# Kernel optimization log

Hardware: AMD Instinct MI355X
Metric: run time of the kernel (lower is better)

The kernel has to match this reference:

```python
import jax, jax.numpy as jnp
import numpy as np

BLOCK = 32          # QLinearLPBQ block_size
W_BITS = 4          # low-precision blockwise weight quantization
ACT_BITS = 16       # ActivationQDQ(bits=16)


def act_qdq(x):
    # per-tensor symmetric 16-bit fake quant-dequant (dynamic absmax scale)
    qmax = 2.0 ** (ACT_BITS - 1) - 1.0  # 32767
    scale = jnp.maximum(jnp.max(jnp.abs(x)) / qmax, 1e-12)
    return jnp.clip(jnp.round(x / scale), -qmax - 1.0, qmax) * scale


def fixed_qdq_u16(x):
    # FixedActivationQDQ: scale = 1/65536, zero_point = 0, unsigned 16-bit grid
    scale = 1.0 / 65536.0
    return jnp.clip(jnp.round(x / scale), 0.0, 65535.0) * scale


def lpbq_dequant(w):
    # blockwise (per output row, per 32-wide input block) 4-bit fake quant-dequant
    O, I = w.shape
    qmax = 2.0 ** (W_BITS - 1) - 1.0  # 7
    wb = w.reshape(O, I // BLOCK, BLOCK)
    s = jnp.maximum(jnp.max(jnp.abs(wb), axis=-1, keepdims=True) / qmax, 1e-12)
    wq = jnp.clip(jnp.round(wb / s), -qmax - 1.0, qmax) * s
    return wq.reshape(O, I)


def setup_inputs() -> dict:
    key = jax.random.key(0)
    k1, k2, k3, k4 = jax.random.split(key, 4)
    B, S, H, I = 2, 4096, 1024, 3072
    x = jax.random.normal(k1, (B, S, H), jnp.float32)
    w_gate = jax.random.normal(k2, (I, H), jnp.float32) * 0.02
    w_up = jax.random.normal(k3, (I, H), jnp.float32) * 0.02
    w_down = jax.random.normal(k4, (H, I), jnp.float32) * 0.02
    return {"x": x, "w_gate": w_gate, "w_up": w_up, "w_down": w_down}


def reference(x, w_gate, w_up, w_down):
    # x: [B, S, H]
    x = act_qdq(x)                                        # up_proj_input_qdq
    up = act_qdq(x @ lpbq_dequant(w_up).T)                # up_proj + output qdq -> [B,S,I]
    gate = act_qdq(x @ lpbq_dequant(w_gate).T)            # gate_proj + output qdq
    sig = fixed_qdq_u16(jax.nn.sigmoid(gate))             # sigmoid on fixed u16 grid
    gate = act_qdq(gate * sig)                            # SiLU (x*sigmoid) + qdq
    o = act_qdq(gate * up)                                # down_proj_input_qdq
    return o @ lpbq_dequant(w_down).T                     # [B, S, H]
```

## Files before the change

### kernel.cpp

```cpp
#include <hip/hip_runtime.h>
#include <hip/hip_bf16.h>
#include <stdint.h>


#define M_ROWS 8192
#define H_DIM 1024
#define I_DIM 3072

typedef unsigned short u16;
typedef unsigned int u32;
typedef __attribute__((ext_vector_type(8))) short bf16x8;
typedef __attribute__((ext_vector_type(4))) float f32x4;

__device__ __forceinline__ float bf2f(u16 v) { return __uint_as_float(((u32)v) << 16); }
__device__ __forceinline__ u16 f2bf(float f) {
  u32 u = __float_as_uint(f);
  u32 r = (u + 0x7fffu + ((u >> 16) & 1u)) >> 16;
  return (u16)r;
}
__device__ __forceinline__ float qdq16i(float x, float inv, float s) {
  float q = rintf(x * inv);
  q = fminf(fmaxf(q, -32768.f), 32767.f);
  return q * s;
}

__device__ __forceinline__ float scale_read(const u32* __restrict__ scal, int s) {
  u32 m = 0;
#pragma unroll
  for (int j = 0; j < 16; ++j) m = max(m, scal[j * 16 + s]);
  return fmaxf(__uint_as_float(m) / 32767.f, 1e-12f);
}

__device__ __forceinline__ void load_lds16(const u16* g, u16* lds) {
  __builtin_amdgcn_global_load_lds(
      (const __attribute__((address_space(1))) u32*)g,
      (__attribute__((address_space(3))) u32*)lds, 16, 0, 0);
}

__device__ __forceinline__ void block_amax_atomic(float mx, u32* scal, int s) {
#pragma unroll
  for (int off = 32; off; off >>= 1) mx = fmaxf(mx, __shfl_xor(mx, off));
  __shared__ float red[4];
  const int lane = threadIdx.x & 63, wave = threadIdx.x >> 6;
  if (lane == 0) red[wave] = mx;
  __syncthreads();
  if (threadIdx.x == 0) {
    float m = fmaxf(fmaxf(red[0], red[1]), fmaxf(red[2], red[3]));
    atomicMax(scal + (blockIdx.x & 15) * 16 + s, __float_as_uint(m));
  }
}

template <int K>
__device__ __forceinline__ void gemm_core(const u16* __restrict__ Ablk,
                                          const u16* __restrict__ Bblk,
                                          f32x4 acc[4][4], u16* smem) {
  u16* As = smem;
  u16* Bs = smem + 4096;
  const int tid = threadIdx.x;
  const int lane = tid & 63, wave = tid >> 6;
  const int wm = wave >> 1, wn = wave & 1;
  const int quad = lane >> 4, mrow = lane & 15;

  const int c0 = tid, c1 = tid + 256;
  const int r0 = c0 >> 2, g0 = ((c0 & 3) ^ ((r0 >> 1) & 3)) * 8;
  const int r1 = c1 >> 2, g1 = ((c1 & 3) ^ ((r1 >> 1) & 3)) * 8;
  const u16* a0 = Ablk + (size_t)r0 * K + g0;
  const u16* a1 = Ablk + (size_t)r1 * K + g1;
  const u16* b0 = Bblk + (size_t)r0 * K + g0;
  const u16* b1 = Bblk + (size_t)r1 * K + g1;
  u16* lA0 = &As[c0 * 8];
  u16* lA1 = &As[c1 * 8];
  u16* lB0 = &Bs[c0 * 8];
  u16* lB1 = &Bs[c1 * 8];

  int aoff[4], boff[4];
  const int lq = (quad ^ ((mrow >> 1) & 3)) * 8;
#pragma unroll
  for (int t = 0; t < 4; ++t) {
    aoff[t] = (wm * 64 + t * 16 + mrow) * 32 + lq;
    boff[t] = (wn * 64 + t * 16 + mrow) * 32 + lq;
  }

  for (int k0 = 0; k0 < K; k0 += 32) {
    __syncthreads();
    load_lds16(a0 + k0, lA0);
    load_lds16(a1 + k0, lA1);
    load_lds16(b0 + k0, lB0);
    load_lds16(b1 + k0, lB1);
    __syncthreads();
    bf16x8 af[4], bfr[4];
#pragma unroll
    for (int t = 0; t < 4; ++t) {
      af[t] = *(const bf16x8*)&As[aoff[t]];
      bfr[t] = *(const bf16x8*)&Bs[boff[t]];
    }
#pragma unroll
    for (int i = 0; i < 4; ++i)
#pragma unroll
      for (int j = 0; j < 4; ++j)
        acc[i][j] = __builtin_amdgcn_mfma_f32_16x16x32_bf16(af[i], bfr[j], acc[i][j], 0, 0, 0);
  }
}

__global__ void __launch_bounds__(256) kgemm1(const u16* __restrict__ xq,
                                              const u16* __restrict__ wcat,
                                              u16* __restrict__ up, u16* __restrict__ gh,
                                              u32* __restrict__ scal) {
  __shared__ __align__(16) u16 smem[8192];
  const int tileN = blockIdx.x * 128;
  const int tileM = blockIdx.y * 128;
  f32x4 acc[4][4];
#pragma unroll
  for (int i = 0; i < 4; ++i)
#pragma unroll
    for (int j = 0; j < 4; ++j) acc[i][j] = (f32x4){0.f, 0.f, 0.f, 0.f};
  gemm_core<H_DIM>(xq + (size_t)tileM * H_DIM, wcat + (size_t)tileN * H_DIM, acc, smem);

  u16* outp;
  int ncol, slot;
  if (tileN < I_DIM) { outp = up; ncol = tileN; slot = 1; }
  else               { outp = gh; ncol = tileN - I_DIM; slot = 2; }

  const int lane = threadIdx.x & 63, wave = threadIdx.x >> 6;
  const int wm = wave >> 1, wn = wave & 1;
  const int rb = (lane >> 4) * 4, cb = lane & 15;
  const int erow = lane >> 2, echk = lane & 3;
  u16* wbase = smem + wave * 1152;
  const u16* rbase = smem + wave * 1152 + erow * 72;
  float mx = 0.f;
#pragma unroll
  for (int i = 0; i < 4; ++i) {
    __syncthreads();
#pragma unroll
    for (int j = 0; j < 4; ++j)
#pragma unroll
      for (int r = 0; r < 4; ++r) {
        float v = acc[i][j][r];
        mx = fmaxf(mx, fabsf(v));
        wbase[(rb + r) * 72 + j * 16 + cb] = f2bf(v);
      }
    __syncthreads();
    uint4 v0 = *(const uint4*)(rbase + echk * 8);
    uint4 v1 = *(const uint4*)(rbase + (echk + 4) * 8);
    size_t grow = (size_t)(tileM + wm * 64 + i * 16 + erow) * I_DIM + (ncol + wn * 64);
    *(uint4*)(outp + grow + echk * 8) = v0;
    *(uint4*)(outp + grow + (echk + 4) * 8) = v1;
  }
  block_amax_atomic(mx, scal, slot);
}

__global__ void __launch_bounds__(256) kgemm2(const u16* __restrict__ oq,
                                              const u16* __restrict__ wdq,
                                              float* __restrict__ out) {
  __shared__ __align__(16) u16 smem[8192];
  const int tileN = blockIdx.x * 128;
  const int tileM = blockIdx.y * 128;
  f32x4 acc[4][4];
#pragma unroll
  for (int i = 0; i < 4; ++i)
#pragma unroll
    for (int j = 0; j < 4; ++j) acc[i][j] = (f32x4){0.f, 0.f, 0.f, 0.f};
  gemm_core<I_DIM>(oq + (size_t)tileM * I_DIM, wdq + (size_t)tileN * I_DIM, acc, smem);

  const int lane = threadIdx.x & 63, wave = threadIdx.x >> 6;
  const int wm = wave >> 1, wn = wave & 1;
  const int rb = (lane >> 4) * 4, cb = lane & 15;
#pragma unroll
  for (int i = 0; i < 4; ++i) {
#pragma unroll
    for (int j = 0; j < 4; ++j) {
      size_t base = (size_t)(tileM + wm * 64 + i * 16 + rb) * H_DIM +
                    (size_t)(tileN + wn * 64 + j * 16 + cb);
#pragma unroll
      for (int r = 0; r < 4; ++r) out[base + (size_t)r * H_DIM] = acc[i][j][r];
    }
  }
}

__global__ void __launch_bounds__(256) kabsmax(const float4* __restrict__ x, int n4,
                                               u32* __restrict__ scal) {
  float mx = 0.f;
  for (int i = blockIdx.x * blockDim.x + threadIdx.x; i < n4; i += gridDim.x * blockDim.x) {
    float4 v = x[i];
    mx = fmaxf(fmaxf(fabsf(v.x), fabsf(v.y)), fmaxf(fmaxf(fabsf(v.z), fabsf(v.w)), mx));
  }
  block_amax_atomic(mx, scal, 0);
}

__global__ void __launch_bounds__(256) kdequant(const float* __restrict__ wu,
                                                const float* __restrict__ wg,
                                                const float* __restrict__ wdn,
                                                u16* __restrict__ wcat, u16* __restrict__ wdq) {
  const int gid = blockIdx.x * 256 + threadIdx.x;
  const int unit = gid >> 3, l8 = gid & 7;
  const float* src;
  u16* dst;
  int u;
  if (unit < 98304)       { src = wu;  dst = wcat;            u = unit; }
  else if (unit < 196608) { src = wg;  dst = wcat + 3145728;  u = unit - 98304; }
  else                    { src = wdn; dst = wdq;             u = unit - 196608; }
  const size_t off = (size_t)u * 32 + (size_t)l8 * 4;
  float4 v = *(const float4*)(src + off);
  float m = fmaxf(fmaxf(fabsf(v.x), fabsf(v.y)), fmaxf(fabsf(v.z), fabsf(v.w)));
  m = fmaxf(m, __shfl_xor(m, 1));
  m = fmaxf(m, __shfl_xor(m, 2));
  m = fmaxf(m, __shfl_xor(m, 4));
  const float s = fmaxf(m / 7.0f, 1e-12f);
  const float inv = 1.0f / s;
  float vv[4] = {v.x, v.y, v.z, v.w};
  u16 o[4];
#pragma unroll
  for (int e = 0; e < 4; ++e) {
    float q = rintf(vv[e] * inv);
    q = fminf(fmaxf(q, -8.f), 7.f);
    o[e] = f2bf(q * s);
  }
  *(ushort4*)(dst + off) = make_ushort4(o[0], o[1], o[2], o[3]);
}

__global__ void __launch_bounds__(256) kqdqx(const float4* __restrict__ x,
                                             ushort4* __restrict__ xq,
                                             const u32* __restrict__ scal) {
  const float s = scale_read(scal, 0);
  const float inv = 1.0f / s;
  const int i = blockIdx.x * 256 + threadIdx.x;
  float4 v = x[i];
  ushort4 o;
  o.x = f2bf(qdq16i(v.x, inv, s));
  o.y = f2bf(qdq16i(v.y, inv, s));
  o.z = f2bf(qdq16i(v.z, inv, s));
  o.w = f2bf(qdq16i(v.w, inv, s));
  xq[i] = o;
}

#define GH4 ((M_ROWS * I_DIM) / 8)
#define EW_BLOCKS 2048

__global__ void __launch_bounds__(256) kswiglu(const uint4* __restrict__ gh,
                                               u32* __restrict__ scal) {
  const float sg = scale_read(scal, 2);
  const float inv = 1.0f / sg;
  float mx = 0.f;
  for (int i = blockIdx.x * 256 + threadIdx.x; i < GH4; i += EW_BLOCKS * 256) {
    union { uint4 v; u16 us[8]; } u;
    u.v = gh[i];
#pragma unroll
    for (int e = 0; e < 8; ++e) {
      float g = qdq16i(bf2f(u.us[e]), inv, sg);
      float sig = __builtin_amdgcn_rcpf(1.f + __expf(-g));
      float sq = fminf(fmaxf(rintf(sig * 65536.f), 0.f), 65535.f) * (1.f / 65536.f);
      mx = fmaxf(mx, fabsf(g * sq));
    }
  }
  block_amax_atomic(mx, scal, 3);
}

__global__ void __launch_bounds__(256) kmulo(uint4* __restrict__ gh, const uint4* __restrict__ up,
                                             u32* __restrict__ scal) {
  const float sg = scale_read(scal, 2);
  const float sh = scale_read(scal, 3);
  const float su = scale_read(scal, 1);
  const float ig = 1.0f / sg, ih = 1.0f / sh, iu = 1.0f / su;
  float mx = 0.f;
  for (int i = blockIdx.x * 256 + threadIdx.x; i < GH4; i += EW_BLOCKS * 256) {
    union { uint4 v; u16 us[8]; } a, b;
    a.v = gh[i];
    b.v = up[i];
#pragma unroll
    for (int e = 0; e < 8; ++e) {
      float g = qdq16i(bf2f(a.us[e]), ig, sg);
      float sig = __builtin_amdgcn_rcpf(1.f + __expf(-g));
      float sq = fminf(fmaxf(rintf(sig * 65536.f), 0.f), 65535.f) * (1.f / 65536.f);
      u16 hb = f2bf(g * sq);
      float o = qdq16i(bf2f(hb), ih, sh) * qdq16i(bf2f(b.us[e]), iu, su);
      mx = fmaxf(mx, fabsf(o));
      a.us[e] = f2bf(o);
    }
    gh[i] = a.v;
  }
  block_amax_atomic(mx, scal, 4);
}

__global__ void __launch_bounds__(256) kqdqo(uint4* __restrict__ gh, const u32* __restrict__ scal) {
  const float so = scale_read(scal, 4);
  const float inv = 1.0f / so;
  const int i = blockIdx.x * 256 + threadIdx.x;
  union { uint4 v; u16 us[8]; } u;
  u.v = gh[i];
#pragma unroll
  for (int e = 0; e < 8; ++e) u.us[e] = f2bf(qdq16i(bf2f(u.us[e]), inv, so));
  gh[i] = u.v;
}

extern "C" void kernel_launch(void* const* d_in, const int* in_sizes, int n_in,
                              void* d_out, int out_size, void* d_ws, size_t ws_size,
                              hipStream_t stream) {
  (void)in_sizes; (void)n_in; (void)out_size; (void)ws_size;
  const float* x   = (const float*)d_in[0];
  const float* wg  = (const float*)d_in[1];
  const float* wu  = (const float*)d_in[2];
  const float* wdn = (const float*)d_in[3];
  float* out = (float*)d_out;
  char* ws = (char*)d_ws;

  u32* scal = (u32*)ws;
  u16* xq   = (u16*)(ws + 1024);
  u16* wcat = xq + (size_t)M_ROWS * H_DIM;
  u16* wdq  = wcat + (size_t)2 * I_DIM * H_DIM;
  u16* up   = wdq + (size_t)H_DIM * I_DIM;
  u16* gh   = up + (size_t)M_ROWS * I_DIM;

  hipMemsetAsync(scal, 0, 1024, stream);
  kabsmax<<<1024, 256, 0, stream>>>((const float4*)x, (M_ROWS * H_DIM) / 4, scal);
  kdequant<<<9216, 256, 0, stream>>>(wu, wg, wdn, wcat, wdq);
  kqdqx<<<(M_ROWS * H_DIM) / 4 / 256, 256, 0, stream>>>((const float4*)x, (ushort4*)xq, scal);
  kgemm1<<<dim3(48, 64), 256, 0, stream>>>(xq, wcat, up, gh, scal);
  kswiglu<<<EW_BLOCKS, 256, 0, stream>>>((const uint4*)gh, scal);
  kmulo<<<EW_BLOCKS, 256, 0, stream>>>((uint4*)gh, (const uint4*)up, scal);
  kqdqo<<<(M_ROWS * I_DIM) / 8 / 256, 256, 0, stream>>>((uint4*)gh, scal);
  kgemm2<<<dim3(8, 64), 256, 0, stream>>>(gh, wdq, out);
}
```

Measured before the change: 375.1 us.

## Fuse SiLU and output amax into gate/up GEMM epilogue, drop elementwise passes

Each GEMM1 block now computes both the gate tile and the matching up tile. The SiLU activation and its absmax are computed in the gate epilogue and kept in a shared-memory buffer, so the up epilogue can also compute the absmax of the gate*up product. This removes the separate swiglu and final-qdq passes over the large intermediate tensors and folds the final quantization into kmulo. It also merges the input absmax and weight dequant kernels into one launch. In exchange, the scales are taken from values before the intermediate quant-dequant steps, which is a slight numeric approximation, and the extra 34 KB of LDS per block may lower GEMM occupancy.

```diff
diff --git a/kernel.cpp b/kernel.cpp
--- a/kernel.cpp
+++ b/kernel.cpp
@@ -22,6 +22,10 @@
   float q = rintf(x * inv);
   q = fminf(fmaxf(q, -32768.f), 32767.f);
   return q * s;
+}
+__device__ __forceinline__ float sigq(float g) {
+  float sig = __builtin_amdgcn_rcpf(1.f + __expf(-g));
+  return fminf(fmaxf(rintf(sig * 65536.f), 0.f), 65535.f) * (1.f / 65536.f);
 }
 
 __device__ __forceinline__ float scale_read(const u32* __restrict__ scal, int s) {
@@ -47,6 +51,25 @@
   if (threadIdx.x == 0) {
     float m = fmaxf(fmaxf(red[0], red[1]), fmaxf(red[2], red[3]));
     atomicMax(scal + (blockIdx.x & 15) * 16 + s, __float_as_uint(m));
+  }
+}
+
+__device__ __forceinline__ void block_amax2(float a, float b, u32* scal, int sa, int sb) {
+#pragma unroll
+  for (int off = 32; off; off >>= 1) {
+    a = fmaxf(a, __shfl_xor(a, off));
+    b = fmaxf(b, __shfl_xor(b, off));
+  }
+  __shared__ float red2[2][4];
+  const int lane = threadIdx.x & 63, wave = threadIdx.x >> 6;
+  if (lane == 0) { red2[0][wave] = a; red2[1][wave] = b; }
+  __syncthreads();
+  if (threadIdx.x == 0) {
+    float ma = fmaxf(fmaxf(red2[0][0], red2[0][1]), fmaxf(red2[0][2], red2[0][3]));
+    float mb = fmaxf(fmaxf(red2[1][0], red2[1][1]), fmaxf(red2[1][2], red2[1][3]));
+    u32* base = scal + (blockIdx.x & 15) * 16;
+    atomicMax(base + sa, __float_as_uint(ma));
+    atomicMax(base + sb, __float_as_uint(mb));
   }
 }
 
@@ -102,51 +125,85 @@
   }
 }
 
+#define HSTRIDE 136
+
 __global__ void __launch_bounds__(256) kgemm1(const u16* __restrict__ xq,
                                               const u16* __restrict__ wcat,
                                               u16* __restrict__ up, u16* __restrict__ gh,
                                               u32* __restrict__ scal) {
   __shared__ __align__(16) u16 smem[8192];
+  __shared__ __align__(16) u16 hbuf[128 * HSTRIDE];
   const int tileN = blockIdx.x * 128;
   const int tileM = blockIdx.y * 128;
-  f32x4 acc[4][4];
-#pragma unroll
-  for (int i = 0; i < 4; ++i)
-#pragma unroll
-    for (int j = 0; j < 4; ++j) acc[i][j] = (f32x4){0.f, 0.f, 0.f, 0.f};
-  gemm_core<H_DIM>(xq + (size_t)tileM * H_DIM, wcat + (size_t)tileN * H_DIM, acc, smem);
-
-  u16* outp;
-  int ncol, slot;
-  if (tileN < I_DIM) { outp = up; ncol = tileN; slot = 1; }
-  else               { outp = gh; ncol = tileN - I_DIM; slot = 2; }
-
   const int lane = threadIdx.x & 63, wave = threadIdx.x >> 6;
   const int wm = wave >> 1, wn = wave & 1;
   const int rb = (lane >> 4) * 4, cb = lane & 15;
   const int erow = lane >> 2, echk = lane & 3;
   u16* wbase = smem + wave * 1152;
-  const u16* rbase = smem + wave * 1152 + erow * 72;
-  float mx = 0.f;
-#pragma unroll
-  for (int i = 0; i < 4; ++i) {
-    __syncthreads();
-#pragma unroll
-    for (int j = 0; j < 4; ++j)
-#pragma unroll
-      for (int r = 0; r < 4; ++r) {
-        float v = acc[i][j][r];
-        mx = fmaxf(mx, fabsf(v));
-        wbase[(rb + r) * 72 + j * 16 + cb] = f2bf(v);
-      }
-    __syncthreads();
-    uint4 v0 = *(const uint4*)(rbase + echk * 8);
-    uint4 v1 = *(const uint4*)(rbase + (echk + 4) * 8);
-    size_t grow = (size_t)(tileM + wm * 64 + i * 16 + erow) * I_DIM + (ncol + wn * 64);
-    *(uint4*)(outp + grow + echk * 8) = v0;
-    *(uint4*)(outp + grow + (echk + 4) * 8) = v1;
-  }
-  block_amax_atomic(mx, scal, slot);
+  const u16* rbase = wbase + erow * 72;
+  const u16* Ablk = xq + (size_t)tileM * H_DIM;
+  f32x4 acc[4][4];
+
+#pragma unroll
+  for (int i = 0; i < 4; ++i)
+#pragma unroll
+    for (int j = 0; j < 4; ++j) acc[i][j] = (f32x4){0.f, 0.f, 0.f, 0.f};
+  gemm_core<H_DIM>(Ablk, wcat + (size_t)(I_DIM + tileN) * H_DIM, acc, smem);
+  {
+    float mxg = 0.f, mxh = 0.f;
+#pragma unroll
+    for (int i = 0; i < 4; ++i) {
+      __syncthreads();
+#pragma unroll
+      for (int j = 0; j < 4; ++j)
+#pragma unroll
+        for (int r = 0; r < 4; ++r) {
+          float g = acc[i][j][r];
+          mxg = fmaxf(mxg, fabsf(g));
+          wbase[(rb + r) * 72 + j * 16 + cb] = f2bf(g);
+          float ha = g * sigq(g);
+          mxh = fmaxf(mxh, fabsf(ha));
+          hbuf[(wm * 64 + i * 16 + rb + r) * HSTRIDE + wn * 64 + j * 16 + cb] = f2bf(ha);
+        }
+      __syncthreads();
+      uint4 v0 = *(const uint4*)(rbase + echk * 8);
+      uint4 v1 = *(const uint4*)(rbase + (echk + 4) * 8);
+      size_t grow = (size_t)(tileM + wm * 64 + i * 16 + erow) * I_DIM + (tileN + wn * 64);
+      *(uint4*)(gh + grow + echk * 8) = v0;
+      *(uint4*)(gh + grow + (echk + 4) * 8) = v1;
+    }
+    block_amax2(mxg, mxh, scal, 2, 3);
+  }
+
+#pragma unroll
+  for (int i = 0; i < 4; ++i)
+#pragma unroll
+    for (int j = 0; j < 4; ++j) acc[i][j] = (f32x4){0.f, 0.f, 0.f, 0.f};
+  gemm_core<H_DIM>(Ablk, wcat + (size_t)tileN * H_DIM, acc, smem);
+  {
+    float mxu = 0.f, mxo = 0.f;
+#pragma unroll
+    for (int i = 0; i < 4; ++i) {
+      __syncthreads();
+#pragma unroll
+      for (int j = 0; j < 4; ++j)
+#pragma unroll
+        for (int r = 0; r < 4; ++r) {
+          float u = acc[i][j][r];
+          mxu = fmaxf(mxu, fabsf(u));
+          wbase[(rb + r) * 72 + j * 16 + cb] = f2bf(u);
+          float ha = bf2f(hbuf[(wm * 64 + i * 16 + rb + r) * HSTRIDE + wn * 64 + j * 16 + cb]);
+          mxo = fmaxf(mxo, fabsf(ha * u));
+        }
+      __syncthreads();
+      uint4 v0 = *(const uint4*)(rbase + echk * 8);
+      uint4 v1 = *(const uint4*)(rbase + (echk + 4) * 8);
+      size_t grow = (size_t)(tileM + wm * 64 + i * 16 + erow) * I_DIM + (tileN + wn * 64);
+      *(uint4*)(up + grow + echk * 8) = v0;
+      *(uint4*)(up + grow + (echk + 4) * 8) = v1;
+    }
+    block_amax2(mxu, mxo, scal, 1, 4);
+  }
 }
 
 __global__ void __launch_bounds__(256) kgemm2(const u16* __restrict__ oq,
@@ -177,21 +234,24 @@
   }
 }
 
-__global__ void __launch_bounds__(256) kabsmax(const float4* __restrict__ x, int n4,
-                                               u32* __restrict__ scal) {
-  float mx = 0.f;
-  for (int i = blockIdx.x * blockDim.x + threadIdx.x; i < n4; i += gridDim.x * blockDim.x) {
-    float4 v = x[i];
-    mx = fmaxf(fmaxf(fabsf(v.x), fabsf(v.y)), fmaxf(fmaxf(fabsf(v.z), fabsf(v.w)), mx));
-  }
-  block_amax_atomic(mx, scal, 0);
-}
-
-__global__ void __launch_bounds__(256) kdequant(const float* __restrict__ wu,
-                                                const float* __restrict__ wg,
-                                                const float* __restrict__ wdn,
-                                                u16* __restrict__ wcat, u16* __restrict__ wdq) {
-  const int gid = blockIdx.x * 256 + threadIdx.x;
+__global__ void __launch_bounds__(256) kprep(const float* __restrict__ x,
+                                             const float* __restrict__ wu,
+                                             const float* __restrict__ wg,
+                                             const float* __restrict__ wdn,
+                                             u16* __restrict__ wcat, u16* __restrict__ wdq,
+                                             u32* __restrict__ scal) {
+  if (blockIdx.x < 1024) {
+    const float4* x4 = (const float4*)x;
+    const int n4 = (M_ROWS * H_DIM) / 4;
+    float mx = 0.f;
+    for (int i = blockIdx.x * 256 + threadIdx.x; i < n4; i += 1024 * 256) {
+      float4 v = x4[i];
+      mx = fmaxf(fmaxf(fabsf(v.x), fabsf(v.y)), fmaxf(fmaxf(fabsf(v.z), fabsf(v.w)), mx));
+    }
+    block_amax_atomic(mx, scal, 0);
+    return;
+  }
+  const int gid = (blockIdx.x - 1024) * 256 + threadIdx.x;
   const int unit = gid >> 3, l8 = gid & 7;
   const float* src;
   u16* dst;
@@ -236,32 +296,12 @@
 #define GH4 ((M_ROWS * I_DIM) / 8)
 #define EW_BLOCKS 2048
 
-__global__ void __launch_bounds__(256) kswiglu(const uint4* __restrict__ gh,
-                                               u32* __restrict__ scal) {
-  const float sg = scale_read(scal, 2);
-  const float inv = 1.0f / sg;
-  float mx = 0.f;
-  for (int i = blockIdx.x * 256 + threadIdx.x; i < GH4; i += EW_BLOCKS * 256) {
-    union { uint4 v; u16 us[8]; } u;
-    u.v = gh[i];
-#pragma unroll
-    for (int e = 0; e < 8; ++e) {
-      float g = qdq16i(bf2f(u.us[e]), inv, sg);
-      float sig = __builtin_amdgcn_rcpf(1.f + __expf(-g));
-      float sq = fminf(fmaxf(rintf(sig * 65536.f), 0.f), 65535.f) * (1.f / 65536.f);
-      mx = fmaxf(mx, fabsf(g * sq));
-    }
-  }
-  block_amax_atomic(mx, scal, 3);
-}
-
 __global__ void __launch_bounds__(256) kmulo(uint4* __restrict__ gh, const uint4* __restrict__ up,
                                              u32* __restrict__ scal) {
-  const float sg = scale_read(scal, 2);
-  const float sh = scale_read(scal, 3);
-  const float su = scale_read(scal, 1);
-  const float ig = 1.0f / sg, ih = 1.0f / sh, iu = 1.0f / su;
-  float mx = 0.f;
+  const float sg = scale_read(scal, 2), ig = 1.0f / sg;
+  const float sh = scale_read(scal, 3), ih = 1.0f / sh;
+  const float su = scale_read(scal, 1), iu = 1.0f / su;
+  const float so = scale_read(scal, 4), io = 1.0f / so;
   for (int i = blockIdx.x * 256 + threadIdx.x; i < GH4; i += EW_BLOCKS * 256) {
     union { uint4 v; u16 us[8]; } a, b;
     a.v = gh[i];
@@ -269,27 +309,12 @@
 #pragma unroll
     for (int e = 0; e < 8; ++e) {
       float g = qdq16i(bf2f(a.us[e]), ig, sg);
-      float sig = __builtin_amdgcn_rcpf(1.f + __expf(-g));
-      float sq = fminf(fmaxf(rintf(sig * 65536.f), 0.f), 65535.f) * (1.f / 65536.f);
-      u16 hb = f2bf(g * sq);
-      float o = qdq16i(bf2f(hb), ih, sh) * qdq16i(bf2f(b.us[e]), iu, su);
-      mx = fmaxf(mx, fabsf(o));
-      a.us[e] = f2bf(o);
+      float h = g * sigq(g);
+      float o = qdq16i(h, ih, sh) * qdq16i(bf2f(b.us[e]), iu, su);
+      a.us[e] = f2bf(qdq16i(o, io, so));
     }
     gh[i] = a.v;
   }
-  block_amax_atomic(mx, scal, 4);
-}
-
-__global__ void __launch_bounds__(256) kqdqo(uint4* __restrict__ gh, const u32* __restrict__ scal) {
-  const float so = scale_read(scal, 4);
-  const float inv = 1.0f / so;
-  const int i = blockIdx.x * 256 + threadIdx.x;
-  union { uint4 v; u16 us[8]; } u;
-  u.v = gh[i];
-#pragma unroll
-  for (int e = 0; e < 8; ++e) u.us[e] = f2bf(qdq16i(bf2f(u.us[e]), inv, so));
-  gh[i] = u.v;
 }
 
 extern "C" void kernel_launch(void* const* d_in, const int* in_sizes, int n_in,
@@ -311,12 +336,9 @@
   u16* gh   = up + (size_t)M_ROWS * I_DIM;
 
   hipMemsetAsync(scal, 0, 1024, stream);
-  kabsmax<<<1024, 256, 0, stream>>>((const float4*)x, (M_ROWS * H_DIM) / 4, scal);
-  kdequant<<<9216, 256, 0, stream>>>(wu, wg, wdn, wcat, wdq);
+  kprep<<<1024 + 9216, 256, 0, stream>>>(x, wu, wg, wdn, wcat, wdq, scal);
   kqdqx<<<(M_ROWS * H_DIM) / 4 / 256, 256, 0, stream>>>((const float4*)x, (ushort4*)xq, scal);
-  kgemm1<<<dim3(48, 64), 256, 0, stream>>>(xq, wcat, up, gh, scal);
-  kswiglu<<<EW_BLOCKS, 256, 0, stream>>>((const uint4*)gh, scal);
+  kgemm1<<<dim3(24, 64), 256, 0, stream>>>(xq, wcat, up, gh, scal);
   kmulo<<<EW_BLOCKS, 256, 0, stream>>>((uint4*)gh, (const uint4*)up, scal);
-  kqdqo<<<(M_ROWS * I_DIM) / 8 / 256, 256, 0, stream>>>((uint4*)gh, scal);
   kgemm2<<<dim3(8, 64), 256, 0, stream>>>(gh, wdq, out);
 }
```

Result: faster. 349.0 us (-7.0%).
